# Optimization experiments

Measured on AMD Instinct MI355X. Metric: run time of the kernel, lower is better.

The kernel has to match this reference:

```python
import jax, jax.numpy as jnp
import numpy as np

N = 32        # fixed segment-tree span in the original module
LEVELS = 5    # log2(N) descent steps (l<r loop runs exactly 5 times)
B, S, D = 16, 8192, 64


def _prefix(x):
    # P[b, m] = sum_{l=1}^{m} x[b, l]  (leaf l holds x[l]; x[0] is never used)
    return jnp.concatenate([jnp.zeros_like(x[:, :1]), jnp.cumsum(x[:, 1:N], axis=1)], axis=1)


def _seg(P, a, b, n, bidx):
    # sum of leaves l in [a, b] with l < n, via prefix sums; shapes a,b,n: [B,S]
    hi = jnp.minimum(b, n - 1)
    ok = hi >= a
    hic = jnp.clip(hi, 0, N - 1)
    v = P[bidx, hic] - P[bidx, a - 1]          # [B,S,D]
    return jnp.where(ok[..., None], v, jnp.zeros((), P.dtype))


def reference(queries, keys, values, valid_lens):
    b, s, d = queries.shape
    if valid_lens is None:
        n = jnp.full((b, s), keys.shape[1], jnp.int32)
    elif valid_lens.ndim == 1:
        n = jnp.broadcast_to(valid_lens.astype(jnp.int32)[:, None], (b, s))
    else:
        n = valid_lens.astype(jnp.int32)
    Pk = _prefix(keys)    # [B,N,D]
    Pv = _prefix(values)  # [B,N,D]
    bidx = jnp.arange(b)[:, None]
    l = jnp.ones((b, s), jnp.int32)
    r = jnp.full((b, s), N, jnp.int32)
    ans = jnp.zeros((b, s, d), queries.dtype)
    for _ in range(LEVELS):
        mid = (l + r) >> 1
        kL = _seg(Pk, l, mid, n, bidx)
        kR = _seg(Pk, mid + 1, r, n, bidx)
        ls = jax.nn.sigmoid(jnp.sum(queries * kL, axis=-1))  # [B,S]
        rs = jax.nn.sigmoid(jnp.sum(queries * kR, axis=-1))
        cond = ls >= rs
        vL = _seg(Pv, l, mid, n, bidx)
        vR = _seg(Pv, mid + 1, r, n, bidx)
        add = jnp.where(cond[..., None], vR * rs[..., None], vL * ls[..., None])
        ans = ans * 0.5 + add
        r = jnp.where(cond, mid, r)
        l = jnp.where(cond, l, mid + 1)
    return ans


def setup_inputs() -> dict:
    key = jax.random.key(0)
    k1, k2, k3, k4 = jax.random.split(key, 4)
    return {
        "queries": jax.random.normal(k1, (B, S, D), jnp.float32),
        "keys": jax.random.normal(k2, (B, N, D), jnp.float32),
        "values": jax.random.normal(k3, (B, N, D), jnp.float32),
        "valid_lens": jax.random.randint(k4, (B,), 0, 32, jnp.int64),
    }
```

## Files before the change

### kernel.cpp

```cpp
#include <hip/hip_runtime.h>
#include <math.h>


#define SEG_N   32
#define DIM     64
#define LEVELS  5
#define QPB     64
#define THREADS 256
#define PAD     68
#define PADB    (PAD * 4)

#define DPP_QUAD_XOR1   0xB1
#define DPP_QUAD_XOR2   0x4E
#define DPP_ROW_HMIRROR 0x141

#if __has_builtin(__builtin_amdgcn_rcpf)
#define RCPF(x) __builtin_amdgcn_rcpf(x)
#else
#define RCPF(x) (1.0f / (x))
#endif

template <int CTRL>
__device__ __forceinline__ float dpp_xadd(float v) {
    const int s = __builtin_amdgcn_update_dpp(0, __float_as_int(v), CTRL, 0xf, 0xf, true);
    return v + __int_as_float(s);
}

__device__ __forceinline__ float group8_sum(float v) {
    v = dpp_xadd<DPP_QUAD_XOR1>(v);
    v = dpp_xadd<DPP_QUAD_XOR2>(v);
    v = dpp_xadd<DPP_ROW_HMIRROR>(v);
    return v;
}

__device__ __forceinline__ float4 f4sub(const float4 a, const float4 b) {
    return make_float4(a.x - b.x, a.y - b.y, a.z - b.z, a.w - b.w);
}
__device__ __forceinline__ float dot4(const float4 a, const float4 b) {
    return a.x * b.x + a.y * b.y + a.z * b.z + a.w * b.w;
}
__device__ __forceinline__ void fma4(float4& acc, const float4 hi, const float4 lo, float w) {
    acc.x = fmaf(hi.x - lo.x, w, acc.x);
    acc.y = fmaf(hi.y - lo.y, w, acc.y);
    acc.z = fmaf(hi.z - lo.z, w, acc.z);
    acc.w = fmaf(hi.w - lo.w, w, acc.w);
}

__global__ __launch_bounds__(THREADS) void segtree_attn_kernel(
    const float* __restrict__ q,
    const float* __restrict__ keys,
    const float* __restrict__ values,
    const int*   __restrict__ vlen,
    float*       __restrict__ out,
    int S)
{
    __shared__ float P[2][SEG_N * PAD];

    const int b = blockIdx.y;
    const int t = threadIdx.x;
    const int g = t >> 3;
    const int u = t & 7;
    const int c = u * 8;
    const int c4 = c * 4;

    const int sA = blockIdx.x * QPB + g;
    const int sB = sA + 32;

    const float* qpA = q + ((size_t)b * S + sA) * DIM + c;
    const float* qpB = q + ((size_t)b * S + sB) * DIM + c;
    const float4 qA0 = *(const float4*)qpA;
    const float4 qA1 = *(const float4*)(qpA + 4);
    const float4 qB0 = *(const float4*)qpB;
    const float4 qB1 = *(const float4*)(qpB + 4);

    if (t < 2 * DIM) {
        const int col = t & (DIM - 1);
        const float* src = ((t < DIM) ? keys : values) + (size_t)b * SEG_N * DIM + col;
        float* dst = (t < DIM) ? P[0] : P[1];
        float acc = 0.0f;
        dst[col] = 0.0f;
        #pragma unroll
        for (int row = 1; row < SEG_N; ++row) {
            acc += src[row * DIM];
            dst[row * PAD + col] = acc;
        }
    }
    const int n = vlen[b];
    __syncthreads();

    const int hnc = max(min(n - 1, SEG_N - 1), 0);
    const float scale[LEVELS] = {0.0625f, 0.125f, 0.25f, 0.5f, 1.0f};
    const char* Kb = (const char*)&P[0][0];
    const char* Vb = (const char*)&P[1][0];

    const int offN = hnc * PADB + c4;
    float4 pkR_A0 = *(const float4*)(Kb + offN);
    float4 pkR_A1 = *(const float4*)(Kb + offN + 16);
    float4 pkR_B0 = pkR_A0, pkR_B1 = pkR_A1;
    float4 pkA_A0 = make_float4(0.f,0.f,0.f,0.f), pkA_A1 = make_float4(0.f,0.f,0.f,0.f);
    float4 pkA_B0 = make_float4(0.f,0.f,0.f,0.f), pkA_B1 = make_float4(0.f,0.f,0.f,0.f);

    int offA_A = c4, offR_A = offN;
    int offA_B = c4, offR_B = offN;
    int midA = 16, midB = 16;
    int lA = 1, rA = SEG_N;
    int lB = 1, rB = SEG_N;

    float wA[LEVELS], wB[LEVELS];
    unsigned int rowsA[LEVELS], rowsB[LEVELS];

    #pragma unroll
    for (int lev = 0; lev < LEVELS; ++lev) {
        const int step = 8 >> lev;
        const int cmA = min(midA, hnc);
        const int cmB = min(midB, hnc);
        const int offMA = cmA * PADB + c4;
        const int offMB = cmB * PADB + c4;

        const float4 pkM_A0 = *(const float4*)(Kb + offMA);
        const float4 pkM_A1 = *(const float4*)(Kb + offMA + 16);
        const float4 pkM_B0 = *(const float4*)(Kb + offMB);
        const float4 pkM_B1 = *(const float4*)(Kb + offMB + 16);

        float dLA = dot4(qA0, f4sub(pkM_A0, pkA_A0)) + dot4(qA1, f4sub(pkM_A1, pkA_A1));
        float dRA = dot4(qA0, f4sub(pkR_A0, pkM_A0)) + dot4(qA1, f4sub(pkR_A1, pkM_A1));
        float dLB = dot4(qB0, f4sub(pkM_B0, pkA_B0)) + dot4(qB1, f4sub(pkM_B1, pkA_B1));
        float dRB = dot4(qB0, f4sub(pkR_B0, pkM_B0)) + dot4(qB1, f4sub(pkR_B1, pkM_B1));

        dLA = group8_sum(dLA);
        dRA = group8_sum(dRA);
        dLB = group8_sum(dLB);
        dRB = group8_sum(dRB);

        const bool okLA = (min(midA, n - 1) >= lA);
        const bool okRA = (min(rA,   n - 1) >= midA + 1);
        const bool okLB = (min(midB, n - 1) >= lB);
        const bool okRB = (min(rB,   n - 1) >= midB + 1);

        const float sLA = okLA ? dLA : 0.0f;
        const float sRA = okRA ? dRA : 0.0f;
        const float sLB = okLB ? dLB : 0.0f;
        const float sRB = okRB ? dRB : 0.0f;

        const float dnLA = 1.0f + __expf(-sLA);
        const float dnRA = 1.0f + __expf(-sRA);
        const float dnLB = 1.0f + __expf(-sLB);
        const float dnRB = 1.0f + __expf(-sRB);

        bool condA = (dnLA <= dnRA);
        bool condB = (dnLB <= dnRB);
        const bool grayA = (dnLA > dnRA) && ((dnLA - dnRA) < dnLA * 1e-6f);
        const bool grayB = (dnLB > dnRB) && ((dnLB - dnRB) < dnLB * 1e-6f);
        if (__any(grayA || grayB)) {
            condA = ((1.0f / dnLA) >= (1.0f / dnRA));
            condB = ((1.0f / dnLB) >= (1.0f / dnRB));
        }

        const bool  okselA = condA ? okRA : okLA;
        const bool  okselB = condB ? okRB : okLB;
        const float wselA  = RCPF(condA ? dnRA : dnLA);
        const float wselB  = RCPF(condB ? dnRB : dnLB);
        wA[lev] = okselA ? (wselA * scale[lev]) : 0.0f;
        wB[lev] = okselB ? (wselB * scale[lev]) : 0.0f;

        const unsigned int hiA = condA ? offR_A : offMA;
        const unsigned int loA = condA ? offMA  : offA_A;
        const unsigned int hiB = condB ? offR_B : offMB;
        const unsigned int loB = condB ? offMB  : offA_B;
        rowsA[lev] = hiA | (loA << 16);
        rowsB[lev] = hiB | (loB << 16);

        if (condA) {
            rA = midA; offR_A = offMA;
            pkR_A0 = pkM_A0; pkR_A1 = pkM_A1;
        } else {
            lA = midA + 1; offA_A = offMA;
            pkA_A0 = pkM_A0; pkA_A1 = pkM_A1;
        }
        if (condB) {
            rB = midB; offR_B = offMB;
            pkR_B0 = pkM_B0; pkR_B1 = pkM_B1;
        } else {
            lB = midB + 1; offA_B = offMB;
            pkA_B0 = pkM_B0; pkA_B1 = pkM_B1;
        }
        if (lev < LEVELS - 1) {
            midA = condA ? (midA - step) : (midA + step);
            midB = condB ? (midB - step) : (midB + step);
        }
    }

    float4 aA0 = make_float4(0.f,0.f,0.f,0.f), aA1 = make_float4(0.f,0.f,0.f,0.f);
    float4 aB0 = make_float4(0.f,0.f,0.f,0.f), aB1 = make_float4(0.f,0.f,0.f,0.f);
    #pragma unroll
    for (int lev = 0; lev < LEVELS; ++lev) {
        const unsigned int pa = rowsA[lev];
        const unsigned int pb = rowsB[lev];
        const unsigned int hiA = pa & 0xFFFFu, loA = pa >> 16;
        const unsigned int hiB = pb & 0xFFFFu, loB = pb >> 16;
        const float4 hA0 = *(const float4*)(Vb + hiA);
        const float4 hA1 = *(const float4*)(Vb + hiA + 16);
        const float4 lA0 = *(const float4*)(Vb + loA);
        const float4 lA1 = *(const float4*)(Vb + loA + 16);
        fma4(aA0, hA0, lA0, wA[lev]);
        fma4(aA1, hA1, lA1, wA[lev]);
        const float4 hB0 = *(const float4*)(Vb + hiB);
        const float4 hB1 = *(const float4*)(Vb + hiB + 16);
        const float4 lB0 = *(const float4*)(Vb + loB);
        const float4 lB1 = *(const float4*)(Vb + loB + 16);
        fma4(aB0, hB0, lB0, wB[lev]);
        fma4(aB1, hB1, lB1, wB[lev]);
    }

    float* opA = out + ((size_t)b * S + sA) * DIM + c;
    float* opB = out + ((size_t)b * S + sB) * DIM + c;
    *(float4*)opA       = aA0;
    *(float4*)(opA + 4) = aA1;
    *(float4*)opB       = aB0;
    *(float4*)(opB + 4) = aB1;
}

extern "C" void kernel_launch(void* const* d_in, const int* in_sizes, int n_in,
                              void* d_out, int out_size, void* d_ws, size_t ws_size,
                              hipStream_t stream) {
    const float* q    = (const float*)d_in[0];
    const float* keys = (const float*)d_in[1];
    const float* vals = (const float*)d_in[2];
    const int*   vl   = (const int*)d_in[3];
    float* out = (float*)d_out;

    const int B = in_sizes[3];
    const int S = in_sizes[0] / (B * DIM);

    dim3 grid(S / QPB, B);
    segtree_attn_kernel<<<grid, THREADS, 0, stream>>>(q, keys, vals, vl, out, S);
}
```

Measured before the change: 24.61 us.

## Telescope value-prefix differences into per-row coefficients to cut LDS reads

Rewrites the weighted sum of prefix-sum differences as a combination of distinct prefix rows. Per-row coefficients are accumulated during the descent, so each boundary row is read once. The value pass drops from 10 to 7 row reads per query, with plain FMAs and no subtracts. The cost is extra select logic and registers in the descent loop, and floating-point summation order changes slightly.

```diff
diff --git a/kernel.cpp b/kernel.cpp
--- a/kernel.cpp
+++ b/kernel.cpp
@@ -39,11 +39,11 @@
 __device__ __forceinline__ float dot4(const float4 a, const float4 b) {
     return a.x * b.x + a.y * b.y + a.z * b.z + a.w * b.w;
 }
-__device__ __forceinline__ void fma4(float4& acc, const float4 hi, const float4 lo, float w) {
-    acc.x = fmaf(hi.x - lo.x, w, acc.x);
-    acc.y = fmaf(hi.y - lo.y, w, acc.y);
-    acc.z = fmaf(hi.z - lo.z, w, acc.z);
-    acc.w = fmaf(hi.w - lo.w, w, acc.w);
+__device__ __forceinline__ void fmaw(float4& acc, const float4 v, float w) {
+    acc.x = fmaf(v.x, w, acc.x);
+    acc.y = fmaf(v.y, w, acc.y);
+    acc.z = fmaf(v.z, w, acc.z);
+    acc.w = fmaf(v.w, w, acc.w);
 }
 
 __global__ __launch_bounds__(THREADS) void segtree_attn_kernel(
@@ -102,12 +102,14 @@
 
     int offA_A = c4, offR_A = offN;
     int offA_B = c4, offR_B = offN;
+    float cA_A = 0.0f, cR_A = 0.0f;
+    float cA_B = 0.0f, cR_B = 0.0f;
     int midA = 16, midB = 16;
     int lA = 1, rA = SEG_N;
     int lB = 1, rB = SEG_N;
 
-    float wA[LEVELS], wB[LEVELS];
-    unsigned int rowsA[LEVELS], rowsB[LEVELS];
+    float cE_A[LEVELS + 2], cE_B[LEVELS + 2];
+    int   rowE_A[LEVELS + 2], rowE_B[LEVELS + 2];
 
     #pragma unroll
     for (int lev = 0; lev < LEVELS; ++lev) {
@@ -160,28 +162,35 @@
         const bool  okselB = condB ? okRB : okLB;
         const float wselA  = RCPF(condA ? dnRA : dnLA);
         const float wselB  = RCPF(condB ? dnRB : dnLB);
-        wA[lev] = okselA ? (wselA * scale[lev]) : 0.0f;
-        wB[lev] = okselB ? (wselB * scale[lev]) : 0.0f;
-
-        const unsigned int hiA = condA ? offR_A : offMA;
-        const unsigned int loA = condA ? offMA  : offA_A;
-        const unsigned int hiB = condB ? offR_B : offMB;
-        const unsigned int loB = condB ? offMB  : offA_B;
-        rowsA[lev] = hiA | (loA << 16);
-        rowsB[lev] = hiB | (loB << 16);
+        const float wAv = okselA ? (wselA * scale[lev]) : 0.0f;
+        const float wBv = okselB ? (wselB * scale[lev]) : 0.0f;
+
+        rowE_A[lev] = condA ? offR_A : offA_A;
+        cE_A[lev]   = condA ? (cR_A + wAv) : (cA_A - wAv);
+        rowE_B[lev] = condB ? offR_B : offA_B;
+        cE_B[lev]   = condB ? (cR_B + wBv) : (cA_B - wBv);
+
+        cR_A   = condA ? -wAv  : cR_A;
+        cA_A   = condA ? cA_A  : wAv;
+        offR_A = condA ? offMA : offR_A;
+        offA_A = condA ? offA_A : offMA;
+        cR_B   = condB ? -wBv  : cR_B;
+        cA_B   = condB ? cA_B  : wBv;
+        offR_B = condB ? offMB : offR_B;
+        offA_B = condB ? offA_B : offMB;
 
         if (condA) {
-            rA = midA; offR_A = offMA;
+            rA = midA;
             pkR_A0 = pkM_A0; pkR_A1 = pkM_A1;
         } else {
-            lA = midA + 1; offA_A = offMA;
+            lA = midA + 1;
             pkA_A0 = pkM_A0; pkA_A1 = pkM_A1;
         }
         if (condB) {
-            rB = midB; offR_B = offMB;
+            rB = midB;
             pkR_B0 = pkM_B0; pkR_B1 = pkM_B1;
         } else {
-            lB = midB + 1; offA_B = offMB;
+            lB = midB + 1;
             pkA_B0 = pkM_B0; pkA_B1 = pkM_B1;
         }
         if (lev < LEVELS - 1) {
@@ -190,26 +199,23 @@
         }
     }
 
+    rowE_A[LEVELS]     = offA_A;  cE_A[LEVELS]     = cA_A;
+    rowE_A[LEVELS + 1] = offR_A;  cE_A[LEVELS + 1] = cR_A;
+    rowE_B[LEVELS]     = offA_B;  cE_B[LEVELS]     = cA_B;
+    rowE_B[LEVELS + 1] = offR_B;  cE_B[LEVELS + 1] = cR_B;
+
     float4 aA0 = make_float4(0.f,0.f,0.f,0.f), aA1 = make_float4(0.f,0.f,0.f,0.f);
     float4 aB0 = make_float4(0.f,0.f,0.f,0.f), aB1 = make_float4(0.f,0.f,0.f,0.f);
     #pragma unroll
-    for (int lev = 0; lev < LEVELS; ++lev) {
-        const unsigned int pa = rowsA[lev];
-        const unsigned int pb = rowsB[lev];
-        const unsigned int hiA = pa & 0xFFFFu, loA = pa >> 16;
-        const unsigned int hiB = pb & 0xFFFFu, loB = pb >> 16;
-        const float4 hA0 = *(const float4*)(Vb + hiA);
-        const float4 hA1 = *(const float4*)(Vb + hiA + 16);
-        const float4 lA0 = *(const float4*)(Vb + loA);
-        const float4 lA1 = *(const float4*)(Vb + loA + 16);
-        fma4(aA0, hA0, lA0, wA[lev]);
-        fma4(aA1, hA1, lA1, wA[lev]);
-        const float4 hB0 = *(const float4*)(Vb + hiB);
-        const float4 hB1 = *(const float4*)(Vb + hiB + 16);
-        const float4 lB0 = *(const float4*)(Vb + loB);
-        const float4 lB1 = *(const float4*)(Vb + loB + 16);
-        fma4(aB0, hB0, lB0, wB[lev]);
-        fma4(aB1, hB1, lB1, wB[lev]);
+    for (int e = 0; e < LEVELS + 2; ++e) {
+        const float4 vA0 = *(const float4*)(Vb + rowE_A[e]);
+        const float4 vA1 = *(const float4*)(Vb + rowE_A[e] + 16);
+        fmaw(aA0, vA0, cE_A[e]);
+        fmaw(aA1, vA1, cE_A[e]);
+        const float4 vB0 = *(const float4*)(Vb + rowE_B[e]);
+        const float4 vB1 = *(const float4*)(Vb + rowE_B[e] + 16);
+        fmaw(aB0, vB0, cE_B[e]);
+        fmaw(aB1, vB1, cE_B[e]);
     }
 
     float* opA = out + ((size_t)b * S + sA) * DIM + c;
```

After: 23.93 us. 2.8% less time.
